# Kernel optimization log

Measured on AMD Instinct MI355X. Metric: run time of the kernel, lower is better.

The kernel has to match this reference:

```python
import jax, jax.numpy as jnp
import numpy as np

B, N, E = 8, 1000, 16000
HIST, PRED = 8, 12
IN_DIM = 14          # pm25(1) + met features(13)
HID_GAT, HEADS = 256, 8
GNN_OUT = 13
HID = 64             # GRU hidden (self.hid_dim = 64 in source)


def setup_inputs() -> dict:
    key = jax.random.key(0)
    ks = jax.random.split(key, 20)
    p = lambda k, shp, s=0.05: jax.random.normal(k, shp, dtype=jnp.float32) * s
    return {
        "pm25_hist": jax.random.normal(ks[0], (B, HIST, N, 1), dtype=jnp.float32),
        "feature": jax.random.normal(ks[1], (B, HIST + PRED, N, IN_DIM - 1), dtype=jnp.float32),
        "edge_index": jax.random.randint(ks[2], (2, E), 0, N),
        "gat1_W": p(ks[3], (IN_DIM, HEADS * HID_GAT)),
        "gat1_att_src": p(ks[4], (HEADS, HID_GAT)),
        "gat1_att_dst": p(ks[5], (HEADS, HID_GAT)),
        "gat1_b": p(ks[6], (HEADS * HID_GAT,)),
        "gat2_W": p(ks[7], (HEADS * HID_GAT, GNN_OUT)),
        "gat2_att_src": p(ks[8], (1, GNN_OUT)),
        "gat2_att_dst": p(ks[9], (1, GNN_OUT)),
        "gat2_b": p(ks[10], (GNN_OUT,)),
        "gru_W_ih": p(ks[11], (3 * HID, IN_DIM + GNN_OUT)),
        "gru_W_hh": p(ks[12], (3 * HID, HID)),
        "gru_b_ih": p(ks[13], (3 * HID,)),
        "gru_b_hh": p(ks[14], (3 * HID,)),
        "fc_out_W": p(ks[15], (HID, 1)),
        "fc_out_b": p(ks[16], (1,)),
    }


def _gat_conv(x, W, a_src, a_dst, b, src, dst, concat):
    # Single-graph GATConv (PyG semantics, eval mode: dropout disabled).
    # x: [N, F_in]; src/dst: [E'] (self-loops already appended)
    H, D = a_src.shape
    h = (x @ W).reshape(N, H, D)                       # [N, H, D]
    e = jax.nn.leaky_relu(
        (h * a_src).sum(-1)[src] + (h * a_dst).sum(-1)[dst], 0.2
    )                                                  # [E', H]
    # segment softmax over incoming edges of each dst node
    m = jax.ops.segment_max(e, dst, num_segments=N)
    ex = jnp.exp(e - m[dst])
    alpha = ex / jax.ops.segment_sum(ex, dst, num_segments=N)[dst]
    out = jax.ops.segment_sum(alpha[:, :, None] * h[src], dst, num_segments=N)  # [N, H, D]
    return (out.reshape(N, H * D) + b) if concat else (out.mean(1) + b)


def reference(pm25_hist, feature, edge_index,
              gat1_W, gat1_att_src, gat1_att_dst, gat1_b,
              gat2_W, gat2_att_src, gat2_att_dst, gat2_b,
              gru_W_ih, gru_W_hh, gru_b_ih, gru_b_hh,
              fc_out_W, fc_out_b):
    # add self-loops (PyG GATConv default)
    loop = jnp.arange(N)
    src = jnp.concatenate([edge_index[0], loop])
    dst = jnp.concatenate([edge_index[1], loop])

    def gnn(x):  # x: [N, IN_DIM] -> [N, GNN_OUT]
        h = jax.nn.elu(_gat_conv(x, gat1_W, gat1_att_src, gat1_att_dst, gat1_b, src, dst, True))
        return _gat_conv(h, gat2_W, gat2_att_src, gat2_att_dst, gat2_b, src, dst, False)

    gnn_b = jax.vmap(gnn)

    def gru(x, h):  # torch.nn.GRUCell math
        i_r, i_z, i_n = jnp.split(x @ gru_W_ih.T + gru_b_ih, 3, axis=-1)
        h_r, h_z, h_n = jnp.split(h @ gru_W_hh.T + gru_b_hh, 3, axis=-1)
        r = jax.nn.sigmoid(i_r + h_r)
        z = jax.nn.sigmoid(i_z + h_z)
        n = jnp.tanh(i_n + r * h_n)
        return (1.0 - z) * n + z * h

    feats = jnp.moveaxis(feature[:, HIST:HIST + PRED], 1, 0)  # [PRED, B, N, 13]

    def step(carry, f_t):
        hn, xn = carry
        x = jnp.concatenate([xn, f_t], axis=-1)               # [B, N, IN_DIM]
        g = gnn_b(x)                                          # [B, N, GNN_OUT]
        gx = jnp.concatenate([g, x], axis=-1).reshape(B * N, IN_DIM + GNN_OUT)
        hn = gru(gx, hn)                                      # [B*N, HID]
        xn = hn.reshape(B, N, HID) @ fc_out_W + fc_out_b      # [B, N, 1]
        return (hn, xn), xn

    h0 = jnp.zeros((B * N, HID), jnp.float32)
    xn0 = pm25_hist[:, -1]                                    # [B, N, 1]
    _, preds = jax.lax.scan(step, (h0, xn0), feats)
    return jnp.moveaxis(preds, 0, 1)                          # [B, PRED, N, 1]
```

## Files before the change

### kernel.cpp

```cpp
#include <hip/hip_runtime.h>
#include <hip/hip_bf16.h>
#include <math.h>

#define BB 8
#define NN 1000
#define EE 16000
#define ETOT 17000
#define TPRED 12
#define FEAT 13
#define INDIM 14
#define HEADS 8
#define HG 256
#define C1 2048
#define GO 13
#define HID 64

typedef unsigned int  uint32;
typedef unsigned short ushort16;
typedef uint32 uvec4 __attribute__((ext_vector_type(4)));
typedef __fp16 hf2 __attribute__((ext_vector_type(2)));

union U32H2 { uint32 u; hf2 h; };
__device__ __forceinline__ hf2 u2h(uint32 u){ U32H2 c; c.u=u; return c.h; }
__device__ __forceinline__ uint32 h2u(hf2 h){ U32H2 c; c.h=h; return c.u; }

#if __has_builtin(__builtin_amdgcn_fdot2)
__device__ __forceinline__ float FDOT2(hf2 a, hf2 b, float c){
    return __builtin_amdgcn_fdot2(a, b, c, false);
}
#else
__device__ __forceinline__ float FDOT2(hf2 a, hf2 b, float c){
    return c + (float)a.x*(float)b.x + (float)a.y*(float)b.y;
}
#endif

__device__ __forceinline__ float lrelu(float v){ return v > 0.f ? v : 0.2f*v; }

__device__ __forceinline__ ushort16 f2bf(float f){
    union { float f; uint32 u; } v; v.f = f;
    uint32 r = v.u + 0x7FFFu + ((v.u >> 16) & 1u);
    return (ushort16)(r >> 16);
}
__device__ __forceinline__ uint32 pack2(float lo, float hi){
    return (uint32)f2bf(lo) | ((uint32)f2bf(hi) << 16);
}
__device__ __forceinline__ void cvt2(uint32 u, float& lo, float& hi){
    union { uint32 u; float f; } a, b;
    a.u = u << 16; b.u = u & 0xFFFF0000u;
    lo = a.f; hi = b.f;
}
__device__ __forceinline__ uint32 pkh(float lo, float hi){
    hf2 h; h.x = (__fp16)lo; h.y = (__fp16)hi; return h2u(h);
}


__global__ void k_att1pre(const float* W1, const float* asrc, const float* adst,
                          float* Wsrc, float* Wdst){
    int k = blockIdx.x >> 3, h = blockIdx.x & 7;
    int tid = threadIdx.x;
    float wv = W1[k*C1 + h*HG + tid];
    float ps = wv * asrc[h*HG + tid];
    float pd = wv * adst[h*HG + tid];
    #pragma unroll
    for (int m=1;m<64;m<<=1){ ps += __shfl_xor(ps,m); pd += __shfl_xor(pd,m); }
    __shared__ float rs[4], rd[4];
    int w = tid>>6;
    if ((tid&63)==0){ rs[w]=ps; rd[w]=pd; }
    __syncthreads();
    if (tid==0){
        Wsrc[k*8+h] = rs[0]+rs[1]+rs[2]+rs[3];
        Wdst[k*8+h] = rd[0]+rd[1]+rd[2]+rd[3];
    }
}

__global__ void k_packW1(const float* W1, uint32* w1pk){
    int i = blockIdx.x*blockDim.x + threadIdx.x;
    if (i < C1*8){
        int c = i >> 3, kk = i & 7;
        float lo = (kk < 7) ? W1[(2*kk)*C1 + c]   : 0.f;
        float hi = (kk < 7) ? W1[(2*kk+1)*C1 + c] : 0.f;
        w1pk[i] = h2u(__builtin_amdgcn_cvt_pkrtz(lo, hi));
    }
}

__global__ void k_att2pre(const float* W2, const float* a2s, const float* a2d,
                          uint32* w2pk){
    int m = blockIdx.x*blockDim.x + threadIdx.x;
    if (m < C1/2){
        int c0 = 2*m, c1 = 2*m+1;
        float colA[16], colB[16];
        float ssA=0.f, ddA=0.f, ssB=0.f, ddB=0.f;
        #pragma unroll
        for (int j=0;j<GO;j++){
            float wA = W2[c0*GO+j], wB = W2[c1*GO+j];
            colA[j]=wA; colB[j]=wB;
            ssA += wA*a2s[j]; ddA += wA*a2d[j];
            ssB += wB*a2s[j]; ddB += wB*a2d[j];
        }
        colA[13]=ssA; colA[14]=ddA; colA[15]=0.f;
        colB[13]=ssB; colB[14]=ddB; colB[15]=0.f;
        #pragma unroll
        for (int j=0;j<16;j++)
            w2pk[m*16+j] = h2u(__builtin_amdgcn_cvt_pkrtz(colA[j], colB[j]));
    }
}

__global__ void k_packGRU(const float* Wih, const float* Whh,
                          uint32* WihP, uint32* WhhP){
    int i = blockIdx.x*blockDim.x + threadIdx.x;
    if (i < 192*14){
        int rr = i/14, c2 = i - rr*14;
        float lo = Wih[rr*27 + 2*c2];
        float hi = (2*c2+1 < 27) ? Wih[rr*27 + 2*c2 + 1] : 0.f;
        WihP[i] = pkh(lo, hi);
    }
    if (i < 192*32){
        int rr = i>>5, j2 = i&31;
        WhhP[i] = pkh(Whh[rr*64 + 2*j2], Whh[rr*64 + 2*j2 + 1]);
    }
}

__global__ void k_init(const float* pm25, const float* feat,
                       const float* Wsrc, const float* Wdst,
                       float* hn, float* xn, int* count,
                       float* ssrc, float* sdst, uint32* xpk){
    int i = blockIdx.x*blockDim.x + threadIdx.x;
    if (i < BB*NN*HID) hn[i] = 0.f;
    if (i < NN) count[i] = 0;
    if (i < BB*NN){
        int b = i/NN, n = i%NN;
        float x[INDIM];
        x[0] = pm25[(b*8 + 7)*NN + n];
        xn[i] = x[0];
        const float* fp = feat + ((size_t)(b*20 + 8)*NN + n)*FEAT;
        #pragma unroll
        for (int k=0;k<FEAT;k++) x[k+1] = fp[k];
        #pragma unroll
        for (int h=0;h<8;h++){
            float ss=0.f, dd=0.f;
            #pragma unroll
            for (int k=0;k<INDIM;k++){ ss += x[k]*Wsrc[k*8+h]; dd += x[k]*Wdst[k*8+h]; }
            ssrc[i*8+h] = ss; sdst[i*8+h] = dd;
        }
        #pragma unroll
        for (int p=0;p<7;p++) xpk[i*8+p] = pack2(x[2*p], x[2*p+1]);
        xpk[i*8+7] = 0u;
    }
}

__global__ void k_count(const int* ei, int* count){
    int e = blockIdx.x*blockDim.x + threadIdx.x;
    if (e < ETOT){
        int dst = (e<EE) ? ei[EE+e] : (e-EE);
        atomicAdd(&count[dst], 1);
    }
}

__global__ void k_scan(const int* count, int* offs, int* cursor){
    __shared__ int s[1024];
    int tid = threadIdx.x;
    int myc = (tid<NN) ? count[tid] : 0;
    s[tid] = myc;
    __syncthreads();
    for (int d=1; d<1024; d<<=1){
        int v = (tid>=d) ? s[tid-d] : 0;
        __syncthreads();
        s[tid] += v;
        __syncthreads();
    }
    if (tid<NN){
        int off = s[tid] - myc;
        offs[tid] = off; cursor[tid] = off;
    }
    if (tid==NN-1) offs[NN] = s[tid];
}

__global__ void k_fill(const int* ei, int* cursor, int* csr_src){
    int e = blockIdx.x*blockDim.x + threadIdx.x;
    if (e < ETOT){
        int src = (e<EE) ? ei[e]    : (e-EE);
        int dst = (e<EE) ? ei[EE+e] : (e-EE);
        int pos = atomicAdd(&cursor[dst], 1);
        csr_src[pos] = src;
    }
}


__global__ __launch_bounds__(64) void k_agg14(const uint32* xpk, const float* ssrc,
        const float* sdst, const int* offs, const int* csr, float* agg){
    int lane = threadIdx.x;
    int blk = blockIdx.x;
    int b = blk & 7, dstn = blk >> 3;
    int bn = b*NN + dstn;
    int base = offs[dstn], deg = offs[dstn+1]-base;
    int slot = lane >> 3, h = lane & 7;
    float sdd = sdst[bn*8 + h];
    float mloc = -1e30f;
    for (int i=slot;i<deg;i+=8){
        int s = csr[base+i];
        mloc = fmaxf(mloc, lrelu(ssrc[(b*NN+s)*8+h]+sdd));
    }
    mloc = fmaxf(mloc, __shfl_xor(mloc,8));
    mloc = fmaxf(mloc, __shfl_xor(mloc,16));
    mloc = fmaxf(mloc, __shfl_xor(mloc,32));
    float dloc = 0.f;
    for (int i=slot;i<deg;i+=8){
        int s = csr[base+i];
        dloc += __expf(lrelu(ssrc[(b*NN+s)*8+h]+sdd)-mloc);
    }
    dloc += __shfl_xor(dloc,8); dloc += __shfl_xor(dloc,16); dloc += __shfl_xor(dloc,32);
    float rden = 1.f/dloc;
    float acc[14];
    #pragma unroll
    for (int k=0;k<14;k++) acc[k]=0.f;
    for (int i=slot;i<deg;i+=8){
        int s = csr[base+i];
        float al = __expf(lrelu(ssrc[(b*NN+s)*8+h]+sdd)-mloc)*rden;
        const uint32* xp = xpk + (size_t)(b*NN+s)*8;
        #pragma unroll
        for (int p=0;p<7;p++){
            float x0,x1; cvt2(xp[p],x0,x1);
            acc[2*p]   += al*x0;
            acc[2*p+1] += al*x1;
        }
    }
    #pragma unroll
    for (int k=0;k<14;k++){
        acc[k] += __shfl_xor(acc[k],8);
        acc[k] += __shfl_xor(acc[k],16);
        acc[k] += __shfl_xor(acc[k],32);
    }
    if (slot==0){
        float* ag = agg + (size_t)bn*128 + h*16;
        #pragma unroll
        for (int p=0;p<7;p++){
            float2 st; st.x = acc[2*p]; st.y = acc[2*p+1];
            *(float2*)(ag + 2*p) = st;
        }
    }
}

__global__ __launch_bounds__(256,1) void k_expand(const float* agg, const uint32* w1pk,
        const uint32* w2pk, const float* b1, float* h2o, float* s2s, float* s2d){
    int tid = threadIdx.x;
    int hh = tid >> 5;
    uint32 w1r[64];
    #pragma unroll
    for (int q=0;q<16;q++){
        uvec4 u = *(const uvec4*)(w1pk + tid*64 + 4*q);
        w1r[4*q]=u.x; w1r[4*q+1]=u.y; w1r[4*q+2]=u.z; w1r[4*q+3]=u.w;
    }
    uint32 w2r[64];
    #pragma unroll
    for (int q=0;q<16;q++){
        uvec4 u = *(const uvec4*)(w2pk + tid*64 + 4*q);
        w2r[4*q]=u.x; w2r[4*q+1]=u.y; w2r[4*q+2]=u.z; w2r[4*q+3]=u.w;
    }
    float b1r[8];
    #pragma unroll
    for (int j=0;j<8;j++) b1r[j] = b1[8*tid+j];
    __shared__ float sred[256*17];
    __shared__ float red2[64];
    for (int idx = blockIdx.x; idx < BB*NN; idx += gridDim.x){
        const float4* ap = (const float4*)(agg + (size_t)idx*128 + hh*16);
        float4 A0=ap[0], A1=ap[1], A2=ap[2], A3=ap[3];
        hf2 agh[7];
        agh[0]=__builtin_amdgcn_cvt_pkrtz(A0.x,A0.y);
        agh[1]=__builtin_amdgcn_cvt_pkrtz(A0.z,A0.w);
        agh[2]=__builtin_amdgcn_cvt_pkrtz(A1.x,A1.y);
        agh[3]=__builtin_amdgcn_cvt_pkrtz(A1.z,A1.w);
        agh[4]=__builtin_amdgcn_cvt_pkrtz(A2.x,A2.y);
        agh[5]=__builtin_amdgcn_cvt_pkrtz(A2.z,A2.w);
        agh[6]=__builtin_amdgcn_cvt_pkrtz(A3.x,A3.y);
        float v[8];
        #pragma unroll
        for (int j=0;j<8;j++){
            float s = b1r[j];
            #pragma unroll
            for (int kk=0;kk<7;kk++) s = FDOT2(agh[kk], u2h(w1r[j*8+kk]), s);
            v[j] = s > 0.f ? s : __expf(s) - 1.f;
        }
        hf2 vp[4];
        #pragma unroll
        for (int q=0;q<4;q++) vp[q] = __builtin_amdgcn_cvt_pkrtz(v[2*q], v[2*q+1]);
        #pragma unroll
        for (int j=0;j<16;j++){
            float s = 0.f;
            #pragma unroll
            for (int q=0;q<4;q++) s = FDOT2(vp[q], u2h(w2r[q*16+j]), s);
            sred[tid*17 + j] = s;
        }
        __syncthreads();
        int j = tid & 15, g = tid >> 4;
        float s = 0.f;
        #pragma unroll
        for (int i=0;i<16;i++) s += sred[(g + 16*i)*17 + j];
        s += __shfl_xor(s, 16);
        s += __shfl_xor(s, 32);
        int lane = tid & 63, w = tid >> 6;
        if (lane < 16) red2[w*16 + lane] = s;
        __syncthreads();
        if (tid < 15){
            float r = red2[tid] + red2[16+tid] + red2[32+tid] + red2[48+tid];
            if (tid < GO)      h2o[idx*GO + tid] = r;
            else if (tid==13)  s2s[idx] = r;
            else               s2d[idx] = r;
        }
        __syncthreads();
    }
}

__global__ __launch_bounds__(64,2) void k_tail(int t, int last,
        const float* feat, const int* offs, const int* csr,
        const float* h2, const float* s2src, const float* s2dst, const float* b2,
        const uint32* WihP, const uint32* WhhP, const float* bih, const float* bhh,
        const float* fcw, const float* fcb, const float* Wsrc, const float* Wdst,
        float* hn, float* xn, float* out,
        float* ssrc, float* sdst, uint32* xpk){
    int lane = threadIdx.x;
    uint32 wih0[14], wih1[14], wih2[14];
    #pragma unroll
    for (int q=0;q<14;q++){
        wih0[q]=WihP[lane*14+q];
        wih1[q]=WihP[(64+lane)*14+q];
        wih2[q]=WihP[(128+lane)*14+q];
    }
    uint32 whh0[32], whh1[32], whh2[32];
    #pragma unroll
    for (int q=0;q<32;q++){
        whh0[q]=WhhP[lane*32+q];
        whh1[q]=WhhP[(64+lane)*32+q];
        whh2[q]=WhhP[(128+lane)*32+q];
    }
    float bi0=bih[lane], bi1=bih[64+lane], bi2=bih[128+lane];
    float bh0=bhh[lane], bh1=bhh[64+lane], bh2=bhh[128+lane];
    float fw = fcw[lane], fb = fcb[0];
    float b2r[GO];
    #pragma unroll
    for (int c=0;c<GO;c++) b2r[c] = b2[c];
    __shared__ uint32 hsP[32];
    for (int r=0;r<4;r++){
        int bn = blockIdx.x*4 + r;
        int b = bn/NN, n = bn - b*NN;
        int base = offs[n], deg = offs[n+1]-base;
        float sdd = s2dst[bn];
        float mloc = -1e30f;
        for (int e=lane;e<deg;e+=64){
            int s = csr[base+e];
            mloc = fmaxf(mloc, lrelu(s2src[b*NN+s] + sdd));
        }
        #pragma unroll
        for (int m=1;m<64;m<<=1) mloc = fmaxf(mloc, __shfl_xor(mloc,m));
        float dloc = 0.f;
        for (int e=lane;e<deg;e+=64){
            int s = csr[base+e];
            dloc += __expf(lrelu(s2src[b*NN+s] + sdd) - mloc);
        }
        #pragma unroll
        for (int m=1;m<64;m<<=1) dloc += __shfl_xor(dloc,m);
        float rdv = 1.f / dloc;
        float acc[GO];
        #pragma unroll
        for (int c=0;c<GO;c++) acc[c]=0.f;
        for (int e=lane;e<deg;e+=64){
            int s = csr[base+e];
            float al = __expf(lrelu(s2src[b*NN+s] + sdd) - mloc) * rdv;
            const float* hr2 = h2 + (size_t)(b*NN+s)*GO;
            #pragma unroll
            for (int c=0;c<GO;c++) acc[c] += al*hr2[c];
        }
        #pragma unroll
        for (int c=0;c<GO;c++){
            #pragma unroll
            for (int m=1;m<64;m<<=1) acc[c] += __shfl_xor(acc[c],m);
        }
        float xnv = xn[bn];
        const float* fp = feat + ((size_t)(b*20 + 8 + t)*NN + n)*FEAT;
        float ft[FEAT];
        #pragma unroll
        for (int k=0;k<FEAT;k++) ft[k] = fp[k];
        hf2 gx[14];
        #pragma unroll
        for (int p=0;p<6;p++)
            gx[p] = u2h(pkh(acc[2*p]+b2r[2*p], acc[2*p+1]+b2r[2*p+1]));
        gx[6] = u2h(pkh(acc[12]+b2r[12], xnv));
        #pragma unroll
        for (int p=0;p<6;p++)
            gx[7+p] = u2h(pkh(ft[2*p], ft[2*p+1]));
        gx[13] = u2h(pkh(ft[12], 0.f));
        float hold = hn[bn*HID + lane];
        if (lane<32) hsP[lane] = pkh(hn[bn*HID + 2*lane], hn[bn*HID + 2*lane + 1]);
        __syncthreads();
        float ir = bi0, iz = bi1, inn = bi2;
        #pragma unroll
        for (int c2=0;c2<14;c2++){
            ir  = FDOT2(gx[c2], u2h(wih0[c2]), ir);
            iz  = FDOT2(gx[c2], u2h(wih1[c2]), iz);
            inn = FDOT2(gx[c2], u2h(wih2[c2]), inn);
        }
        float hr = bh0, hz = bh1, hnv = bh2;
        #pragma unroll
        for (int j2=0;j2<32;j2++){
            hf2 hv = u2h(hsP[j2]);
            hr  = FDOT2(hv, u2h(whh0[j2]), hr);
            hz  = FDOT2(hv, u2h(whh1[j2]), hz);
            hnv = FDOT2(hv, u2h(whh2[j2]), hnv);
        }
        float rg = 1.f/(1.f+__expf(-(ir+hr)));
        float zg = 1.f/(1.f+__expf(-(iz+hz)));
        float nv = tanhf(inn + rg*hnv);
        float hnew = (1.f - zg)*nv + zg*hold;
        hn[bn*HID+lane] = hnew;
        float xv = hnew * fw;
        #pragma unroll
        for (int m=1;m<64;m<<=1) xv += __shfl_xor(xv,m);
        float res = xv + fb;
        if (lane==0){
            xn[bn] = res;
            out[(b*TPRED + t)*NN + n] = res;
        }
        if (!last){
            const float* fp2 = feat + ((size_t)(b*20 + 9 + t)*NN + n)*FEAT;
            if (lane < 16){
                int h = lane & 7;
                const float* Wa = (lane<8) ? Wsrc : Wdst;
                float s = res * Wa[h];
                #pragma unroll
                for (int k=1;k<14;k++) s += fp2[k-1]*Wa[k*8+h];
                if (lane<8) ssrc[bn*8+h] = s; else sdst[bn*8+h] = s;
            } else if (lane < 23){
                int p = lane - 16;
                float lo = (p==0) ? res : fp2[2*p-1];
                float hi = fp2[2*p];
                xpk[bn*8+p] = pack2(lo, hi);
            } else if (lane == 23){
                xpk[bn*8+7] = 0u;
            }
        }
        __syncthreads();
    }
}


extern "C" void kernel_launch(void* const* d_in, const int* in_sizes, int n_in,
                              void* d_out, int out_size, void* d_ws, size_t ws_size,
                              hipStream_t stream){
    const float* pm25 = (const float*)d_in[0];
    const float* feat = (const float*)d_in[1];
    const int*   ei   = (const int*)  d_in[2];
    const float* W1   = (const float*)d_in[3];
    const float* a1s  = (const float*)d_in[4];
    const float* a1d  = (const float*)d_in[5];
    const float* b1   = (const float*)d_in[6];
    const float* W2   = (const float*)d_in[7];
    const float* a2s  = (const float*)d_in[8];
    const float* a2d  = (const float*)d_in[9];
    const float* b2   = (const float*)d_in[10];
    const float* Wih  = (const float*)d_in[11];
    const float* Whh  = (const float*)d_in[12];
    const float* bih  = (const float*)d_in[13];
    const float* bhh  = (const float*)d_in[14];
    const float* fcw  = (const float*)d_in[15];
    const float* fcb  = (const float*)d_in[16];
    float* out = (float*)d_out;

    float* f = (float*)d_ws;
    size_t o = 0;
    float* ssrc1 = f+o; o += (size_t)BB*NN*8;
    float* sdst1 = f+o; o += (size_t)BB*NN*8;
    float* agg   = f+o; o += (size_t)BB*NN*128;
    float* h2    = f+o; o += (size_t)BB*NN*GO + 8;
    float* s2s   = f+o; o += (size_t)BB*NN;
    float* s2d   = f+o; o += (size_t)BB*NN;
    float* hn    = f+o; o += (size_t)BB*NN*HID;
    float* xn    = f+o; o += (size_t)BB*NN;
    float* Wsrc  = f+o; o += INDIM*8;
    float* Wdst  = f+o; o += INDIM*8;
    uint32* xpk  = (uint32*)(f+o); o += (size_t)BB*NN*8;
    uint32* w1pk = (uint32*)(f+o); o += (size_t)C1*8;
    uint32* w2pk = (uint32*)(f+o); o += (size_t)(C1/2)*16;
    uint32* WihP = (uint32*)(f+o); o += 192*14;
    uint32* WhhP = (uint32*)(f+o); o += 192*32;
    int* ibase  = (int*)(f+o);
    int* count  = ibase;
    int* cursor = ibase + NN;
    int* offs   = ibase + 2*NN;
    int* csr    = ibase + 2*NN + NN + 1;

    k_att1pre<<<112, 256,0,stream>>>(W1, a1s, a1d, Wsrc, Wdst);
    k_packW1 <<<64,  256,0,stream>>>(W1, w1pk);
    k_att2pre<<<4,   256,0,stream>>>(W2, a2s, a2d, w2pk);
    k_packGRU<<<24,  256,0,stream>>>(Wih, Whh, WihP, WhhP);
    k_init   <<<2000,256,0,stream>>>(pm25, feat, Wsrc, Wdst, hn, xn, count,
                                     ssrc1, sdst1, xpk);
    k_count  <<<67,  256,0,stream>>>(ei, count);
    k_scan   <<<1,  1024,0,stream>>>(count, offs, cursor);
    k_fill   <<<67,  256,0,stream>>>(ei, cursor, csr);

    for (int t=0; t<TPRED; t++){
        k_agg14  <<<8000, 64,0,stream>>>(xpk, ssrc1, sdst1, offs, csr, agg);
        k_expand <<<512, 256,0,stream>>>(agg, w1pk, w2pk, b1, h2, s2s, s2d);
        k_tail   <<<2000, 64,0,stream>>>(t, (t==TPRED-1)?1:0, feat, offs, csr,
                                         h2, s2s, s2d, b2,
                                         WihP, WhhP, bih, bhh, fcw, fcb, Wsrc, Wdst,
                                         hn, xn, out, ssrc1, sdst1, xpk);
    }
}
```

Measured before the change: 835.8 us.

## Fuse GAT aggregation into expand kernel, merge prep kernels, re-parallelize tail aggregation

Merges the four weight-packing kernels into one launch. Fuses the layer-1 edge aggregation into the expand kernel, so each 256-thread block aggregates four nodes per round into shared memory and then expands them, removing the agg buffer's global round trip and one launch per timestep. Restructures the layer-2 aggregation in the tail kernel so each of 16 lanes handles one output channel across 4 edge slots, replacing 13 full-wave shuffle reductions with two shuffle steps. The fused kernel adds extra __syncthreads per node and keeps large register arrays, which may limit occupancy.

```diff
diff --git a/kernel.cpp b/kernel.cpp
--- a/kernel.cpp
+++ b/kernel.cpp
@@ -53,70 +53,64 @@
     hf2 h; h.x = (__fp16)lo; h.y = (__fp16)hi; return h2u(h);
 }
 
-
-__global__ void k_att1pre(const float* W1, const float* asrc, const float* adst,
-                          float* Wsrc, float* Wdst){
-    int k = blockIdx.x >> 3, h = blockIdx.x & 7;
-    int tid = threadIdx.x;
-    float wv = W1[k*C1 + h*HG + tid];
-    float ps = wv * asrc[h*HG + tid];
-    float pd = wv * adst[h*HG + tid];
-    #pragma unroll
-    for (int m=1;m<64;m<<=1){ ps += __shfl_xor(ps,m); pd += __shfl_xor(pd,m); }
+__global__ void k_prep(const float* W1, const float* a1s, const float* a1d,
+                       const float* W2, const float* a2s, const float* a2d,
+                       const float* Wih, const float* Whh,
+                       float* Wsrc, float* Wdst, uint32* w1pk, uint32* w2pk,
+                       uint32* WihP, uint32* WhhP){
     __shared__ float rs[4], rd[4];
-    int w = tid>>6;
-    if ((tid&63)==0){ rs[w]=ps; rd[w]=pd; }
-    __syncthreads();
-    if (tid==0){
-        Wsrc[k*8+h] = rs[0]+rs[1]+rs[2]+rs[3];
-        Wdst[k*8+h] = rd[0]+rd[1]+rd[2]+rd[3];
-    }
-}
-
-__global__ void k_packW1(const float* W1, uint32* w1pk){
-    int i = blockIdx.x*blockDim.x + threadIdx.x;
-    if (i < C1*8){
+    int bid = blockIdx.x, tid = threadIdx.x;
+    if (bid < 112){
+        int k = bid >> 3, h = bid & 7;
+        float wv = W1[k*C1 + h*HG + tid];
+        float ps = wv * a1s[h*HG + tid];
+        float pd = wv * a1d[h*HG + tid];
+        #pragma unroll
+        for (int m=1;m<64;m<<=1){ ps += __shfl_xor(ps,m); pd += __shfl_xor(pd,m); }
+        int w = tid>>6;
+        if ((tid&63)==0){ rs[w]=ps; rd[w]=pd; }
+        __syncthreads();
+        if (tid==0){
+            Wsrc[k*8+h] = rs[0]+rs[1]+rs[2]+rs[3];
+            Wdst[k*8+h] = rd[0]+rd[1]+rd[2]+rd[3];
+        }
+    } else if (bid < 176){
+        int i = (bid-112)*256 + tid;
         int c = i >> 3, kk = i & 7;
         float lo = (kk < 7) ? W1[(2*kk)*C1 + c]   : 0.f;
         float hi = (kk < 7) ? W1[(2*kk+1)*C1 + c] : 0.f;
         w1pk[i] = h2u(__builtin_amdgcn_cvt_pkrtz(lo, hi));
-    }
-}
-
-__global__ void k_att2pre(const float* W2, const float* a2s, const float* a2d,
-                          uint32* w2pk){
-    int m = blockIdx.x*blockDim.x + threadIdx.x;
-    if (m < C1/2){
-        int c0 = 2*m, c1 = 2*m+1;
-        float colA[16], colB[16];
-        float ssA=0.f, ddA=0.f, ssB=0.f, ddB=0.f;
-        #pragma unroll
-        for (int j=0;j<GO;j++){
-            float wA = W2[c0*GO+j], wB = W2[c1*GO+j];
-            colA[j]=wA; colB[j]=wB;
-            ssA += wA*a2s[j]; ddA += wA*a2d[j];
-            ssB += wB*a2s[j]; ddB += wB*a2d[j];
-        }
-        colA[13]=ssA; colA[14]=ddA; colA[15]=0.f;
-        colB[13]=ssB; colB[14]=ddB; colB[15]=0.f;
-        #pragma unroll
-        for (int j=0;j<16;j++)
-            w2pk[m*16+j] = h2u(__builtin_amdgcn_cvt_pkrtz(colA[j], colB[j]));
-    }
-}
-
-__global__ void k_packGRU(const float* Wih, const float* Whh,
-                          uint32* WihP, uint32* WhhP){
-    int i = blockIdx.x*blockDim.x + threadIdx.x;
-    if (i < 192*14){
-        int rr = i/14, c2 = i - rr*14;
-        float lo = Wih[rr*27 + 2*c2];
-        float hi = (2*c2+1 < 27) ? Wih[rr*27 + 2*c2 + 1] : 0.f;
-        WihP[i] = pkh(lo, hi);
-    }
-    if (i < 192*32){
-        int rr = i>>5, j2 = i&31;
-        WhhP[i] = pkh(Whh[rr*64 + 2*j2], Whh[rr*64 + 2*j2 + 1]);
+    } else if (bid < 180){
+        int m = (bid-176)*256 + tid;
+        if (m < C1/2){
+            int c0 = 2*m, c1 = 2*m+1;
+            float colA[16], colB[16];
+            float ssA=0.f, ddA=0.f, ssB=0.f, ddB=0.f;
+            #pragma unroll
+            for (int j=0;j<GO;j++){
+                float wA = W2[c0*GO+j], wB = W2[c1*GO+j];
+                colA[j]=wA; colB[j]=wB;
+                ssA += wA*a2s[j]; ddA += wA*a2d[j];
+                ssB += wB*a2s[j]; ddB += wB*a2d[j];
+            }
+            colA[13]=ssA; colA[14]=ddA; colA[15]=0.f;
+            colB[13]=ssB; colB[14]=ddB; colB[15]=0.f;
+            #pragma unroll
+            for (int j=0;j<16;j++)
+                w2pk[m*16+j] = h2u(__builtin_amdgcn_cvt_pkrtz(colA[j], colB[j]));
+        }
+    } else {
+        int i = (bid-180)*256 + tid;
+        if (i < 192*14){
+            int rr = i/14, c2 = i - rr*14;
+            float lo = Wih[rr*27 + 2*c2];
+            float hi = (2*c2+1 < 27) ? Wih[rr*27 + 2*c2 + 1] : 0.f;
+            WihP[i] = pkh(lo, hi);
+        }
+        if (i < 192*32){
+            int rr = i>>5, j2 = i&31;
+            WhhP[i] = pkh(Whh[rr*64 + 2*j2], Whh[rr*64 + 2*j2 + 1]);
+        }
     }
 }
 
@@ -186,63 +180,12 @@
 }
 
 
-__global__ __launch_bounds__(64) void k_agg14(const uint32* xpk, const float* ssrc,
-        const float* sdst, const int* offs, const int* csr, float* agg){
-    int lane = threadIdx.x;
-    int blk = blockIdx.x;
-    int b = blk & 7, dstn = blk >> 3;
-    int bn = b*NN + dstn;
-    int base = offs[dstn], deg = offs[dstn+1]-base;
-    int slot = lane >> 3, h = lane & 7;
-    float sdd = sdst[bn*8 + h];
-    float mloc = -1e30f;
-    for (int i=slot;i<deg;i+=8){
-        int s = csr[base+i];
-        mloc = fmaxf(mloc, lrelu(ssrc[(b*NN+s)*8+h]+sdd));
-    }
-    mloc = fmaxf(mloc, __shfl_xor(mloc,8));
-    mloc = fmaxf(mloc, __shfl_xor(mloc,16));
-    mloc = fmaxf(mloc, __shfl_xor(mloc,32));
-    float dloc = 0.f;
-    for (int i=slot;i<deg;i+=8){
-        int s = csr[base+i];
-        dloc += __expf(lrelu(ssrc[(b*NN+s)*8+h]+sdd)-mloc);
-    }
-    dloc += __shfl_xor(dloc,8); dloc += __shfl_xor(dloc,16); dloc += __shfl_xor(dloc,32);
-    float rden = 1.f/dloc;
-    float acc[14];
-    #pragma unroll
-    for (int k=0;k<14;k++) acc[k]=0.f;
-    for (int i=slot;i<deg;i+=8){
-        int s = csr[base+i];
-        float al = __expf(lrelu(ssrc[(b*NN+s)*8+h]+sdd)-mloc)*rden;
-        const uint32* xp = xpk + (size_t)(b*NN+s)*8;
-        #pragma unroll
-        for (int p=0;p<7;p++){
-            float x0,x1; cvt2(xp[p],x0,x1);
-            acc[2*p]   += al*x0;
-            acc[2*p+1] += al*x1;
-        }
-    }
-    #pragma unroll
-    for (int k=0;k<14;k++){
-        acc[k] += __shfl_xor(acc[k],8);
-        acc[k] += __shfl_xor(acc[k],16);
-        acc[k] += __shfl_xor(acc[k],32);
-    }
-    if (slot==0){
-        float* ag = agg + (size_t)bn*128 + h*16;
-        #pragma unroll
-        for (int p=0;p<7;p++){
-            float2 st; st.x = acc[2*p]; st.y = acc[2*p+1];
-            *(float2*)(ag + 2*p) = st;
-        }
-    }
-}
-
-__global__ __launch_bounds__(256,1) void k_expand(const float* agg, const uint32* w1pk,
-        const uint32* w2pk, const float* b1, float* h2o, float* s2s, float* s2d){
+__global__ __launch_bounds__(256) void k_gnn(const uint32* xpk, const float* ssrc,
+        const float* sdst, const int* offs, const int* csr,
+        const uint32* w1pk, const uint32* w2pk, const float* b1,
+        float* h2o, float* s2s, float* s2d){
     int tid = threadIdx.x;
+    int w = tid >> 6, lane = tid & 63;
     int hh = tid >> 5;
     uint32 w1r[64];
     #pragma unroll
@@ -259,52 +202,111 @@
     float b1r[8];
     #pragma unroll
     for (int j=0;j<8;j++) b1r[j] = b1[8*tid+j];
+    __shared__ float aggL[4][128];
     __shared__ float sred[256*17];
     __shared__ float red2[64];
-    for (int idx = blockIdx.x; idx < BB*NN; idx += gridDim.x){
-        const float4* ap = (const float4*)(agg + (size_t)idx*128 + hh*16);
-        float4 A0=ap[0], A1=ap[1], A2=ap[2], A3=ap[3];
-        hf2 agh[7];
-        agh[0]=__builtin_amdgcn_cvt_pkrtz(A0.x,A0.y);
-        agh[1]=__builtin_amdgcn_cvt_pkrtz(A0.z,A0.w);
-        agh[2]=__builtin_amdgcn_cvt_pkrtz(A1.x,A1.y);
-        agh[3]=__builtin_amdgcn_cvt_pkrtz(A1.z,A1.w);
-        agh[4]=__builtin_amdgcn_cvt_pkrtz(A2.x,A2.y);
-        agh[5]=__builtin_amdgcn_cvt_pkrtz(A2.z,A2.w);
-        agh[6]=__builtin_amdgcn_cvt_pkrtz(A3.x,A3.y);
-        float v[8];
-        #pragma unroll
-        for (int j=0;j<8;j++){
-            float s = b1r[j];
+    for (int rr=0; rr<4; rr++){
+        int nid = rr*2048 + w*512 + blockIdx.x;
+        if (nid < BB*NN){
+            int b = nid & 7, dstn = nid >> 3;
+            int bn = b*NN + dstn;
+            int base = offs[dstn], deg = offs[dstn+1]-base;
+            int slot = lane >> 3, h = lane & 7;
+            float sdd = sdst[bn*8 + h];
+            float mloc = -1e30f;
+            for (int i=slot;i<deg;i+=8){
+                int s = csr[base+i];
+                mloc = fmaxf(mloc, lrelu(ssrc[(b*NN+s)*8+h]+sdd));
+            }
+            mloc = fmaxf(mloc, __shfl_xor(mloc,8));
+            mloc = fmaxf(mloc, __shfl_xor(mloc,16));
+            mloc = fmaxf(mloc, __shfl_xor(mloc,32));
+            float dloc = 0.f;
+            for (int i=slot;i<deg;i+=8){
+                int s = csr[base+i];
+                dloc += __expf(lrelu(ssrc[(b*NN+s)*8+h]+sdd)-mloc);
+            }
+            dloc += __shfl_xor(dloc,8); dloc += __shfl_xor(dloc,16); dloc += __shfl_xor(dloc,32);
+            float rden = 1.f/dloc;
+            float acc[14];
             #pragma unroll
-            for (int kk=0;kk<7;kk++) s = FDOT2(agh[kk], u2h(w1r[j*8+kk]), s);
-            v[j] = s > 0.f ? s : __expf(s) - 1.f;
-        }
-        hf2 vp[4];
-        #pragma unroll
-        for (int q=0;q<4;q++) vp[q] = __builtin_amdgcn_cvt_pkrtz(v[2*q], v[2*q+1]);
-        #pragma unroll
-        for (int j=0;j<16;j++){
-            float s = 0.f;
+            for (int k=0;k<14;k++) acc[k]=0.f;
+            for (int i=slot;i<deg;i+=8){
+                int s = csr[base+i];
+                float al = __expf(lrelu(ssrc[(b*NN+s)*8+h]+sdd)-mloc)*rden;
+                const uint32* xp = xpk + (size_t)(b*NN+s)*8;
+                #pragma unroll
+                for (int p=0;p<7;p++){
+                    float x0,x1; cvt2(xp[p],x0,x1);
+                    acc[2*p]   += al*x0;
+                    acc[2*p+1] += al*x1;
+                }
+            }
             #pragma unroll
-            for (int q=0;q<4;q++) s = FDOT2(vp[q], u2h(w2r[q*16+j]), s);
-            sred[tid*17 + j] = s;
-        }
-        __syncthreads();
-        int j = tid & 15, g = tid >> 4;
-        float s = 0.f;
-        #pragma unroll
-        for (int i=0;i<16;i++) s += sred[(g + 16*i)*17 + j];
-        s += __shfl_xor(s, 16);
-        s += __shfl_xor(s, 32);
-        int lane = tid & 63, w = tid >> 6;
-        if (lane < 16) red2[w*16 + lane] = s;
-        __syncthreads();
-        if (tid < 15){
-            float r = red2[tid] + red2[16+tid] + red2[32+tid] + red2[48+tid];
-            if (tid < GO)      h2o[idx*GO + tid] = r;
-            else if (tid==13)  s2s[idx] = r;
-            else               s2d[idx] = r;
+            for (int k=0;k<14;k++){
+                acc[k] += __shfl_xor(acc[k],8);
+                acc[k] += __shfl_xor(acc[k],16);
+                acc[k] += __shfl_xor(acc[k],32);
+            }
+            if (slot==0){
+                float* ag = &aggL[w][h*16];
+                #pragma unroll
+                for (int k=0;k<14;k++) ag[k] = acc[k];
+            }
+        }
+        __syncthreads();
+        #pragma unroll
+        for (int i=0;i<4;i++){
+            int nid2 = rr*2048 + i*512 + blockIdx.x;
+            if (nid2 < BB*NN){
+                int b2i = nid2 & 7, d2 = nid2 >> 3;
+                int bn2 = b2i*NN + d2;
+                const float4* ap = (const float4*)(&aggL[i][hh*16]);
+                float4 A0=ap[0], A1=ap[1], A2=ap[2], A3=ap[3];
+                hf2 agh[7];
+                agh[0]=__builtin_amdgcn_cvt_pkrtz(A0.x,A0.y);
+                agh[1]=__builtin_amdgcn_cvt_pkrtz(A0.z,A0.w);
+                agh[2]=__builtin_amdgcn_cvt_pkrtz(A1.x,A1.y);
+                agh[3]=__builtin_amdgcn_cvt_pkrtz(A1.z,A1.w);
+                agh[4]=__builtin_amdgcn_cvt_pkrtz(A2.x,A2.y);
+                agh[5]=__builtin_amdgcn_cvt_pkrtz(A2.z,A2.w);
+                agh[6]=__builtin_amdgcn_cvt_pkrtz(A3.x,A3.y);
+                float v[8];
+                #pragma unroll
+                for (int j=0;j<8;j++){
+                    float s = b1r[j];
+                    #pragma unroll
+                    for (int kk=0;kk<7;kk++) s = FDOT2(agh[kk], u2h(w1r[j*8+kk]), s);
+                    v[j] = s > 0.f ? s : __expf(s) - 1.f;
+                }
+                hf2 vp[4];
+                #pragma unroll
+                for (int q=0;q<4;q++) vp[q] = __builtin_amdgcn_cvt_pkrtz(v[2*q], v[2*q+1]);
+                #pragma unroll
+                for (int j=0;j<16;j++){
+                    float s = 0.f;
+                    #pragma unroll
+                    for (int q=0;q<4;q++) s = FDOT2(vp[q], u2h(w2r[q*16+j]), s);
+                    sred[tid*17 + j] = s;
+                }
+                __syncthreads();
+                int j = tid & 15, g = tid >> 4;
+                float s = 0.f;
+                #pragma unroll
+                for (int q=0;q<16;q++) s += sred[(g + 16*q)*17 + j];
+                s += __shfl_xor(s, 16);
+                s += __shfl_xor(s, 32);
+                int ww = tid >> 6, ll = tid & 63;
+                if (ll < 16) red2[ww*16 + ll] = s;
+                __syncthreads();
+                if (tid < 15){
+                    float rv = red2[tid] + red2[16+tid] + red2[32+tid] + red2[48+tid];
+                    if (tid < GO)      h2o[bn2*GO + tid] = rv;
+                    else if (tid==13)  s2s[bn2] = rv;
+                    else               s2d[bn2] = rv;
+                }
+                __syncthreads();
+            }
         }
         __syncthreads();
     }
@@ -318,6 +320,7 @@
         float* hn, float* xn, float* out,
         float* ssrc, float* sdst, uint32* xpk){
     int lane = threadIdx.x;
+    int slot = lane >> 4, cc = lane & 15;
     uint32 wih0[14], wih1[14], wih2[14];
     #pragma unroll
     for (int q=0;q<14;q++){
@@ -335,62 +338,53 @@
     float bi0=bih[lane], bi1=bih[64+lane], bi2=bih[128+lane];
     float bh0=bhh[lane], bh1=bhh[64+lane], bh2=bhh[128+lane];
     float fw = fcw[lane], fb = fcb[0];
-    float b2r[GO];
-    #pragma unroll
-    for (int c=0;c<GO;c++) b2r[c] = b2[c];
+    float b2c = b2[cc < GO ? cc : 0];
     __shared__ uint32 hsP[32];
+    __shared__ float garr[14];
     for (int r=0;r<4;r++){
         int bn = blockIdx.x*4 + r;
         int b = bn/NN, n = bn - b*NN;
         int base = offs[n], deg = offs[n+1]-base;
         float sdd = s2dst[bn];
         float mloc = -1e30f;
-        for (int e=lane;e<deg;e+=64){
+        for (int e=slot;e<deg;e+=4){
             int s = csr[base+e];
             mloc = fmaxf(mloc, lrelu(s2src[b*NN+s] + sdd));
         }
-        #pragma unroll
-        for (int m=1;m<64;m<<=1) mloc = fmaxf(mloc, __shfl_xor(mloc,m));
+        mloc = fmaxf(mloc, __shfl_xor(mloc,16));
+        mloc = fmaxf(mloc, __shfl_xor(mloc,32));
         float dloc = 0.f;
-        for (int e=lane;e<deg;e+=64){
+        for (int e=slot;e<deg;e+=4){
             int s = csr[base+e];
             dloc += __expf(lrelu(s2src[b*NN+s] + sdd) - mloc);
         }
-        #pragma unroll
-        for (int m=1;m<64;m<<=1) dloc += __shfl_xor(dloc,m);
+        dloc += __shfl_xor(dloc,16);
+        dloc += __shfl_xor(dloc,32);
         float rdv = 1.f / dloc;
-        float acc[GO];
-        #pragma unroll
-        for (int c=0;c<GO;c++) acc[c]=0.f;
-        for (int e=lane;e<deg;e+=64){
+        float a = 0.f;
+        for (int e=slot;e<deg;e+=4){
             int s = csr[base+e];
             float al = __expf(lrelu(s2src[b*NN+s] + sdd) - mloc) * rdv;
-            const float* hr2 = h2 + (size_t)(b*NN+s)*GO;
-            #pragma unroll
-            for (int c=0;c<GO;c++) acc[c] += al*hr2[c];
-        }
-        #pragma unroll
-        for (int c=0;c<GO;c++){
-            #pragma unroll
-            for (int m=1;m<64;m<<=1) acc[c] += __shfl_xor(acc[c],m);
-        }
+            a += al * h2[(size_t)(b*NN+s)*GO + cc];
+        }
+        a += __shfl_xor(a,16);
+        a += __shfl_xor(a,32);
         float xnv = xn[bn];
+        if (slot==0 && cc<GO)  garr[cc] = a + b2c;
+        if (slot==0 && cc==GO) garr[GO] = xnv;
+        float hold = hn[bn*HID + lane];
+        if (lane<32) hsP[lane] = pkh(hn[bn*HID + 2*lane], hn[bn*HID + 2*lane + 1]);
+        __syncthreads();
         const float* fp = feat + ((size_t)(b*20 + 8 + t)*NN + n)*FEAT;
         float ft[FEAT];
         #pragma unroll
         for (int k=0;k<FEAT;k++) ft[k] = fp[k];
         hf2 gx[14];
         #pragma unroll
-        for (int p=0;p<6;p++)
-            gx[p] = u2h(pkh(acc[2*p]+b2r[2*p], acc[2*p+1]+b2r[2*p+1]));
-        gx[6] = u2h(pkh(acc[12]+b2r[12], xnv));
-        #pragma unroll
-        for (int p=0;p<6;p++)
-            gx[7+p] = u2h(pkh(ft[2*p], ft[2*p+1]));
+        for (int p=0;p<7;p++) gx[p] = u2h(pkh(garr[2*p], garr[2*p+1]));
+        #pragma unroll
+        for (int p=0;p<6;p++) gx[7+p] = u2h(pkh(ft[2*p], ft[2*p+1]));
         gx[13] = u2h(pkh(ft[12], 0.f));
-        float hold = hn[bn*HID + lane];
-        if (lane<32) hsP[lane] = pkh(hn[bn*HID + 2*lane], hn[bn*HID + 2*lane + 1]);
-        __syncthreads();
         float ir = bi0, iz = bi1, inn = bi2;
         #pragma unroll
         for (int c2=0;c2<14;c2++){
@@ -468,7 +462,6 @@
     size_t o = 0;
     float* ssrc1 = f+o; o += (size_t)BB*NN*8;
     float* sdst1 = f+o; o += (size_t)BB*NN*8;
-    float* agg   = f+o; o += (size_t)BB*NN*128;
     float* h2    = f+o; o += (size_t)BB*NN*GO + 8;
     float* s2s   = f+o; o += (size_t)BB*NN;
     float* s2d   = f+o; o += (size_t)BB*NN;
@@ -487,22 +480,20 @@
     int* offs   = ibase + 2*NN;
     int* csr    = ibase + 2*NN + NN + 1;
 
-    k_att1pre<<<112, 256,0,stream>>>(W1, a1s, a1d, Wsrc, Wdst);
-    k_packW1 <<<64,  256,0,stream>>>(W1, w1pk);
-    k_att2pre<<<4,   256,0,stream>>>(W2, a2s, a2d, w2pk);
-    k_packGRU<<<24,  256,0,stream>>>(Wih, Whh, WihP, WhhP);
-    k_init   <<<2000,256,0,stream>>>(pm25, feat, Wsrc, Wdst, hn, xn, count,
-                                     ssrc1, sdst1, xpk);
-    k_count  <<<67,  256,0,stream>>>(ei, count);
-    k_scan   <<<1,  1024,0,stream>>>(count, offs, cursor);
-    k_fill   <<<67,  256,0,stream>>>(ei, cursor, csr);
+    k_prep  <<<204, 256,0,stream>>>(W1, a1s, a1d, W2, a2s, a2d, Wih, Whh,
+                                    Wsrc, Wdst, w1pk, w2pk, WihP, WhhP);
+    k_init  <<<2000,256,0,stream>>>(pm25, feat, Wsrc, Wdst, hn, xn, count,
+                                    ssrc1, sdst1, xpk);
+    k_count <<<67,  256,0,stream>>>(ei, count);
+    k_scan  <<<1,  1024,0,stream>>>(count, offs, cursor);
+    k_fill  <<<67,  256,0,stream>>>(ei, cursor, csr);
 
     for (int t=0; t<TPRED; t++){
-        k_agg14  <<<8000, 64,0,stream>>>(xpk, ssrc1, sdst1, offs, csr, agg);
-        k_expand <<<512, 256,0,stream>>>(agg, w1pk, w2pk, b1, h2, s2s, s2d);
-        k_tail   <<<2000, 64,0,stream>>>(t, (t==TPRED-1)?1:0, feat, offs, csr,
-                                         h2, s2s, s2d, b2,
-                                         WihP, WhhP, bih, bhh, fcw, fcb, Wsrc, Wdst,
-                                         hn, xn, out, ssrc1, sdst1, xpk);
-    }
-}
+        k_gnn  <<<512, 256,0,stream>>>(xpk, ssrc1, sdst1, offs, csr,
+                                       w1pk, w2pk, b1, h2, s2s, s2d);
+        k_tail <<<2000, 64,0,stream>>>(t, (t==TPRED-1)?1:0, feat, offs, csr,
+                                       h2, s2s, s2d, b2,
+                                       WihP, WhhP, bih, bhh, fcw, fcb, Wsrc, Wdst,
+                                       hn, xn, out, ssrc1, sdst1, xpk);
+    }
+}
```

Measured after the change: 927.2 us. 1.11x slower.
